# Performance work log

Measured on AMD Instinct MI355X. Metric: run time of the kernel, lower is better.

The kernel has to match this reference:

```python
import jax, jax.numpy as jnp
import numpy as np

DIM = 512
NH, NKV, HD = 8, 4, DIM // 8
KVD = NKV * HD
EPS = 1.1920928955078125e-07  # torch.finfo(float32).eps (F.rms_norm default)
ROPE_BASE = 10000.0


def _rms_norm(x):
    # F.rms_norm over last dim, no learned weight
    ms = jnp.mean(jnp.square(x), axis=-1, keepdims=True)
    return x * jax.lax.rsqrt(ms + EPS)


def _rope_tables(T, dtype):
    inv_freq = 1.0 / (ROPE_BASE ** (jnp.arange(0, HD, 2, dtype=jnp.float32) / HD))
    t = jnp.arange(T, dtype=jnp.float32)
    f = jnp.outer(t, inv_freq)  # [T, HD//2]
    return jnp.cos(f).astype(dtype)[None, None], jnp.sin(f).astype(dtype)[None, None]


def _apply_rot(x, c, s):
    h = x.shape[-1] // 2
    x1, x2 = x[..., :h], x[..., h:]
    return jnp.concatenate((x1 * c + x2 * s, -x1 * s + x2 * c), axis=-1)


def setup_inputs() -> dict:
    key = jax.random.key(0)
    ks = jax.random.split(key, 5)
    B, T = 8, 2048
    x = jax.random.normal(ks[0], (B, T, DIM), dtype=jnp.float32)
    # torch Linear weights: [out_features, in_features]
    Wq = jax.random.normal(ks[1], (DIM, DIM), dtype=jnp.float32) * (DIM ** -0.5)
    Wk = jax.random.normal(ks[2], (KVD, DIM), dtype=jnp.float32) * (DIM ** -0.5)
    Wv = jax.random.normal(ks[3], (KVD, DIM), dtype=jnp.float32) * (DIM ** -0.5)
    Wp = jax.random.normal(ks[4], (DIM, DIM), dtype=jnp.float32) * (DIM ** -0.5)
    return {"x": x, "Wq": Wq, "Wk": Wk, "Wv": Wv, "Wp": Wp}


def reference(x, Wq, Wk, Wv, Wp):
    B, T, C = x.shape
    q = (x @ Wq.T).reshape(B, T, NH, HD).transpose(0, 2, 1, 3)    # [B,NH,T,HD]
    k = (x @ Wk.T).reshape(B, T, NKV, HD).transpose(0, 2, 1, 3)   # [B,NKV,T,HD]
    v = (x @ Wv.T).reshape(B, T, NKV, HD).transpose(0, 2, 1, 3)
    q, k = _rms_norm(q), _rms_norm(k)
    c, s = _rope_tables(T, q.dtype)
    q, k = _apply_rot(q, c, s), _apply_rot(k, c, s)
    rep = NH // NKV
    k = jnp.repeat(k, rep, axis=1)  # GQA expand -> [B,NH,T,HD]
    v = jnp.repeat(v, rep, axis=1)
    scale = 1.0 / jnp.sqrt(jnp.asarray(HD, dtype=q.dtype))
    scores = jnp.einsum('bhqd,bhkd->bhqk', q, k) * scale
    causal = jnp.tril(jnp.ones((T, T), dtype=bool))
    scores = jnp.where(causal[None, None], scores, jnp.finfo(scores.dtype).min)
    attn = jax.nn.softmax(scores, axis=-1)
    y = jnp.einsum('bhqk,bhkd->bhqd', attn, v)
    y = y.transpose(0, 2, 1, 3).reshape(B, T, C)
    return y @ Wp.T
```

## Files before the change

### kernel.cpp

```cpp
#include <hip/hip_runtime.h>
#include <hip/hip_bf16.h>
#include <stdint.h>

typedef __bf16 bf16;
typedef __bf16 bf16x8 __attribute__((ext_vector_type(8)));
typedef __bf16 bf16x4 __attribute__((ext_vector_type(4)));
typedef float f32x4 __attribute__((ext_vector_type(4)));

#define T_SEQ 2048
#define DIM_ 512
#define NH_ 8
#define NKV_ 4
#define HD_ 64
#define BT_ (8 * T_SEQ)
#define NEG_INF (-1e30f)
#define EPS_ 1.1920928955078125e-07f
#define QSCALE 0.18033688011112042f
#define SMAX 12.0f

#define OFF_XB   (size_t)(0)
#define OFF_WQKV (size_t)(16777216)
#define OFF_WP   (size_t)(17825792)
#define OFF_COS  (size_t)(18350080)
#define OFF_SIN  (size_t)(18612224)
#define OFF_QT   (size_t)(18874368)
#define OFF_KT   (size_t)(35651584)
#define OFF_VT   (size_t)(44040192)
#define OFF_Y    (size_t)(52428800)
#define WS_NEEDED (size_t)(69206016)

__device__ inline void mfma16(f32x4& acc, bf16x8 a, bf16x8 b) {
    acc = __builtin_amdgcn_mfma_f32_16x16x32_bf16(a, b, acc, 0, 0, 0);
}

typedef const __attribute__((address_space(1))) uint8_t* gas_ptr;
typedef __attribute__((address_space(3))) uint8_t* las_ptr;
__device__ inline void gload16(const bf16* g, bf16* l) {
    __builtin_amdgcn_global_load_lds((gas_ptr)(const void*)g, (las_ptr)(void*)l, 16, 0, 0);
}

__global__ void prep_kernel(const float* __restrict__ x, const float* __restrict__ wq,
                            const float* __restrict__ wk, const float* __restrict__ wv,
                            const float* __restrict__ wp,
                            bf16* __restrict__ xb, bf16* __restrict__ wqkv,
                            bf16* __restrict__ wpb, float* __restrict__ cosT,
                            float* __restrict__ sinT) {
    int tid = blockIdx.x * blockDim.x + threadIdx.x;
    int stride = gridDim.x * blockDim.x;
    for (int i = tid; i < BT_ * DIM_; i += stride) xb[i] = (bf16)x[i];
    for (int i = tid; i < 1024 * 512; i += stride) {
        int j = i >> 9, k = i & 511;
        float v;
        if (j < 512) v = wq[i];
        else if (j < 768) v = wk[(j - 512) * 512 + k];
        else v = wv[(j - 768) * 512 + k];
        wqkv[i] = (bf16)v;
    }
    for (int i = tid; i < 512 * 512; i += stride) wpb[i] = (bf16)wp[i];
    for (int i = tid; i < T_SEQ * 32; i += stride) {
        int t = i >> 5, d = i & 31;
        float inv = powf(10000.0f, -(float)d * (1.0f / 32.0f));
        float f = (float)t * inv;
        cosT[i] = cosf(f);
        sinT[i] = sinf(f);
    }
}

__global__ __launch_bounds__(256) void qkv_gemm(const bf16* __restrict__ A,
                                                const bf16* __restrict__ B,
                                                bf16* __restrict__ qt,
                                                bf16* __restrict__ kt,
                                                bf16* __restrict__ vt,
                                                const float* __restrict__ cosT,
                                                const float* __restrict__ sinT) {
    __shared__ __align__(16) char smem[34816];
    bf16* As = (bf16*)smem;
    bf16* Bs = (bf16*)(smem + 16384);
    const int tid = threadIdx.x, lane = tid & 63, wid = tid >> 6;
    const int wr = wid >> 1, wc = wid & 1;
    const int lm = lane & 15, hi = lane >> 4;
    const int bid = blockIdx.x;
    const int swz = (bid & 7) * 128 + (bid >> 3);
    const int brow = (swz & 127) * 128;
    const int bcol = (swz >> 7) * 128;

    f32x4 acc[4][4] = {};
    for (int k0 = 0; k0 < 512; k0 += 64) {
        __syncthreads();
#pragma unroll
        for (int i = 0; i < 4; ++i) {
            int c = i * 256 + tid;
            int slot = c >> 6, l = c & 63;
            int row = (slot >> 1) * 16 + (l & 15);
            int kc = (slot & 1) * 32 + (l >> 4) * 8;
            gload16(A + (size_t)(brow + row) * 512 + k0 + kc, As + c * 8);
            gload16(B + (size_t)(bcol + row) * 512 + k0 + kc, Bs + c * 8);
        }
        asm volatile("s_waitcnt vmcnt(0)" ::: "memory");
        __syncthreads();
#pragma unroll
        for (int kk = 0; kk < 2; ++kk) {
            bf16x8 af[4], bfr[4];
#pragma unroll
            for (int m = 0; m < 4; ++m)
                af[m] = *(const bf16x8*)(As + (((wr * 4 + m) * 2 + kk) * 64 + lane) * 8);
#pragma unroll
            for (int n = 0; n < 4; ++n)
                bfr[n] = *(const bf16x8*)(Bs + (((wc * 4 + n) * 2 + kk) * 64 + lane) * 8);
            __builtin_amdgcn_s_setprio(1);
#pragma unroll
            for (int m = 0; m < 4; ++m)
#pragma unroll
                for (int n = 0; n < 4; ++n) mfma16(acc[m][n], af[m], bfr[n]);
            __builtin_amdgcn_s_setprio(0);
        }
    }
    __syncthreads();

    bf16* Tb = (bf16*)smem + wid * 4224;
    const int wcol = bcol + wc * 64;
    const int ctype = (wcol < 512) ? 0 : (wcol < 768 ? 1 : 2);

    if (ctype < 2) {
#pragma unroll
        for (int m = 0; m < 4; ++m)
#pragma unroll
            for (int r = 0; r < 4; ++r) {
                float v0 = acc[m][0][r], v1 = acc[m][1][r];
                float v2 = acc[m][2][r], v3 = acc[m][3][r];
                float ss = v0 * v0 + v1 * v1 + v2 * v2 + v3 * v3;
                ss += __shfl_xor(ss, 1);
                ss += __shfl_xor(ss, 2);
                ss += __shfl_xor(ss, 4);
                ss += __shfl_xor(ss, 8);
                float rinv = rsqrtf(ss * (1.0f / 64.0f) + EPS_);
                v0 *= rinv; v1 *= rinv; v2 *= rinv; v3 *= rinv;
                int rl = m * 16 + hi * 4 + r;
                int t = (brow + wr * 64 + rl) & (T_SEQ - 1);
                float c0 = cosT[t * 32 + lm], s0 = sinT[t * 32 + lm];
                float c1 = cosT[t * 32 + 16 + lm], s1 = sinT[t * 32 + 16 + lm];
                float o0 = v0 * c0 + v2 * s0;
                float o2 = v2 * c0 - v0 * s0;
                float o1 = v1 * c1 + v3 * s1;
                float o3 = v3 * c1 - v1 * s1;
                if (ctype == 0) { o0 *= QSCALE; o1 *= QSCALE; o2 *= QSCALE; o3 *= QSCALE; }
                Tb[rl * 66 + lm]      = (bf16)o0;
                Tb[rl * 66 + 16 + lm] = (bf16)o1;
                Tb[rl * 66 + 32 + lm] = (bf16)o2;
                Tb[rl * 66 + 48 + lm] = (bf16)o3;
            }
    } else {
#pragma unroll
        for (int m = 0; m < 4; ++m)
#pragma unroll
            for (int n = 0; n < 4; ++n)
#pragma unroll
                for (int r = 0; r < 4; ++r)
                    Tb[(n * 16 + lm) * 66 + m * 16 + hi * 4 + r] = (bf16)acc[m][n][r];
    }
    __syncthreads();

    const int i0 = brow + wr * 64;
    const int b = i0 >> 11, tt = i0 & (T_SEQ - 1);
#pragma unroll
    for (int p = 0; p < 8; ++p) {
        int row = p * 8 + (lane >> 3);
        int ch = lane & 7;
        bf16x8 val = *(const bf16x8*)(Tb + row * 66 + ch * 8);
        if (ctype == 0) {
            int head = wcol >> 6;
            *(bf16x8*)(qt + ((size_t)((b << 3) + head) * T_SEQ + tt + row) * 64 + ch * 8) = val;
        } else if (ctype == 1) {
            int head = (wcol - 512) >> 6;
            *(bf16x8*)(kt + ((size_t)((b << 2) + head) * T_SEQ + tt + row) * 64 + ch * 8) = val;
        } else {
            int head = (wcol - 768) >> 6;
            *(bf16x8*)(vt + ((size_t)((b << 2) + head) * 64 + row) * T_SEQ + tt + ch * 8) = val;
        }
    }
}

__global__ __launch_bounds__(256, 4) void attn_kernel(const bf16* __restrict__ qt,
                                                      const bf16* __restrict__ kt,
                                                      const bf16* __restrict__ vt,
                                                      bf16* __restrict__ y) {
    __shared__ bf16 Klds[4096];
    __shared__ bf16 Vlds[4096];
    __shared__ bf16 Plds[4][32 * 40];
    const int tid = threadIdx.x;
    const int lane = tid & 63, wid = tid >> 6;
    const int lm = lane & 15, hi = lane >> 4;
    const int bid = blockIdx.x;
    const int s4 = bid >> 8;
    const int g4 = (bid >> 6) & 3;
    const int bh = bid & 63;
    const int p = 4 * (3 - s4) + ((g4 + s4) & 3);
    const int b = bh >> 3, h = bh & 7, hv = h >> 1;
    const bf16* Q = qt + (size_t)bh * T_SEQ * HD_;
    const bf16* K = kt + (size_t)(b * NKV_ + hv) * T_SEQ * HD_;
    const bf16* V = vt + (size_t)(b * NKV_ + hv) * HD_ * T_SEQ;
    const int qB = p * 128;
    const int qw = qB + wid * 32;
    bf16* Pl = &Plds[wid][0];

    const int sl0 = tid >> 6, l0 = tid & 63;
    const int gr0 = (sl0 >> 1) * 16 + (l0 & 15);
    const int gc0 = (sl0 & 1) * 32 + (l0 >> 4) * 8;
    const int sl1 = (256 + tid) >> 6;
    const int gr1 = (sl1 >> 1) * 16 + (l0 & 15);
    const int gc1 = (sl1 & 1) * 32 + (l0 >> 4) * 8;
    const bf16* kg0 = K + (size_t)gr0 * HD_ + gc0;
    const bf16* kg1 = K + (size_t)gr1 * HD_ + gc1;
    const bf16* vg0 = V + (size_t)gr0 * T_SEQ + gc0;
    const bf16* vg1 = V + (size_t)gr1 * T_SEQ + gc1;
    bf16* kd0 = Klds + (size_t)tid * 8;
    bf16* kd1 = Klds + (size_t)(256 + tid) * 8;
    bf16* vd0 = Vlds + (size_t)tid * 8;
    bf16* vd1 = Vlds + (size_t)(256 + tid) * 8;

    bf16x8 qf[2][2];
#pragma unroll
    for (int qm = 0; qm < 2; ++qm)
#pragma unroll
        for (int kk = 0; kk < 2; ++kk)
            qf[qm][kk] = *(const bf16x8*)(Q + (size_t)(qw + 16 * qm + lm) * HD_ + 32 * kk + 8 * hi);

    f32x4 o[2][4] = {};
    float lrow[2] = {0.f, 0.f};

    const int nt = (qB >> 6) + 2;
    for (int t = 0; t < nt; ++t) {
        const int kv0 = t << 6;
        __syncthreads();
        {
            size_t ko = (size_t)kv0 * HD_, vo = (size_t)kv0;
            gload16(kg0 + ko, kd0);
            gload16(kg1 + ko, kd1);
            gload16(vg0 + vo, vd0);
            gload16(vg1 + vo, vd1);
        }
        asm volatile("s_waitcnt vmcnt(0)" ::: "memory");
        __syncthreads();

        if (kv0 <= qw + 31) {
            f32x4 s[2][4] = {};
#pragma unroll
            for (int kk = 0; kk < 2; ++kk) {
                bf16x8 kf[4];
#pragma unroll
                for (int n = 0; n < 4; ++n)
                    kf[n] = *(const bf16x8*)(Klds + ((n * 2 + kk) * 64 + lane) * 8);
#pragma unroll
                for (int qm = 0; qm < 2; ++qm)
#pragma unroll
                    for (int n = 0; n < 4; ++n) mfma16(s[qm][n], kf[n], qf[qm][kk]);
            }
            const bool partial = (kv0 + 63 > qw);
            bf16x4 pw[2][4];
#pragma unroll
            for (int qm = 0; qm < 2; ++qm) {
                const int qg = qw + 16 * qm + lm;
                float ps = 0.f;
#pragma unroll
                for (int n = 0; n < 4; ++n)
#pragma unroll
                    for (int r = 0; r < 4; ++r) {
                        float xv = s[qm][n][r];
                        if (partial)
                            xv = ((kv0 + 16 * n + 4 * hi + r) <= qg) ? xv : NEG_INF;
                        float e = __builtin_amdgcn_exp2f(xv - SMAX);
                        ps += e;
                        pw[qm][n][r] = (bf16)e;
                    }
                ps += __shfl_xor(ps, 16);
                ps += __shfl_xor(ps, 32);
                lrow[qm] += ps;
            }
#pragma unroll
            for (int kk = 0; kk < 2; ++kk) {
#pragma unroll
                for (int qm = 0; qm < 2; ++qm) {
                    *(bf16x4*)(Pl + (16 * qm + lm) * 40 + 4 * hi)      = pw[qm][2 * kk];
                    *(bf16x4*)(Pl + (16 * qm + lm) * 40 + 16 + 4 * hi) = pw[qm][2 * kk + 1];
                }
                bf16x8 vf[4], pf[2];
#pragma unroll
                for (int qm = 0; qm < 2; ++qm)
                    pf[qm] = *(const bf16x8*)(Pl + (16 * qm + lm) * 40 + 8 * hi);
#pragma unroll
                for (int nd = 0; nd < 4; ++nd)
                    vf[nd] = *(const bf16x8*)(Vlds + ((nd * 2 + kk) * 64 + lane) * 8);
#pragma unroll
                for (int qm = 0; qm < 2; ++qm)
#pragma unroll
                    for (int nd = 0; nd < 4; ++nd) mfma16(o[qm][nd], vf[nd], pf[qm]);
            }
        }
    }

#pragma unroll
    for (int qm = 0; qm < 2; ++qm) {
        float rcl = 1.0f / lrow[qm];
#pragma unroll
        for (int nd = 0; nd < 4; ++nd) {
            bf16x4 ov;
#pragma unroll
            for (int r = 0; r < 4; ++r) ov[r] = (bf16)(o[qm][nd][r] * rcl);
            *(bf16x4*)(Pl + lm * 72 + nd * 16 + 4 * hi) = ov;
        }
#pragma unroll
        for (int it = 0; it < 2; ++it) {
            int chunk = it * 64 + lane;
            int row = chunk >> 3, dc = (chunk & 7) * 8;
            bf16x8 val = *(const bf16x8*)(Pl + row * 72 + dc);
            *(bf16x8*)(y + (size_t)(b * T_SEQ + qw + 16 * qm + row) * DIM_ + h * HD_ + dc) = val;
        }
    }
}

__global__ __launch_bounds__(256) void proj_gemm(const bf16* __restrict__ A,
                                                 const bf16* __restrict__ B,
                                                 float* __restrict__ out) {
    __shared__ __align__(16) char smem[32768];
    bf16* As = (bf16*)smem;
    bf16* Bs = (bf16*)(smem + 16384);
    const int tid = threadIdx.x, lane = tid & 63, wid = tid >> 6;
    const int wr = wid >> 1, wc = wid & 1;
    const int lm = lane & 15, hi = lane >> 4;
    const int bid = blockIdx.x;
    const int swz = (bid & 7) * 64 + (bid >> 3);
    const int brow = (swz & 127) * 128;
    const int bcol = (swz >> 7) * 128;

    f32x4 acc[4][4] = {};
    for (int k0 = 0; k0 < 512; k0 += 64) {
        __syncthreads();
#pragma unroll
        for (int i = 0; i < 4; ++i) {
            int c = i * 256 + tid;
            int slot = c >> 6, l = c & 63;
            int row = (slot >> 1) * 16 + (l & 15);
            int kc = (slot & 1) * 32 + (l >> 4) * 8;
            gload16(A + (size_t)(brow + row) * 512 + k0 + kc, As + c * 8);
            gload16(B + (size_t)(bcol + row) * 512 + k0 + kc, Bs + c * 8);
        }
        asm volatile("s_waitcnt vmcnt(0)" ::: "memory");
        __syncthreads();
#pragma unroll
        for (int kk = 0; kk < 2; ++kk) {
            bf16x8 af[4], bfr[4];
#pragma unroll
            for (int m = 0; m < 4; ++m)
                af[m] = *(const bf16x8*)(As + (((wr * 4 + m) * 2 + kk) * 64 + lane) * 8);
#pragma unroll
            for (int n = 0; n < 4; ++n)
                bfr[n] = *(const bf16x8*)(Bs + (((wc * 4 + n) * 2 + kk) * 64 + lane) * 8);
            __builtin_amdgcn_s_setprio(1);
#pragma unroll
            for (int m = 0; m < 4; ++m)
#pragma unroll
                for (int n = 0; n < 4; ++n) mfma16(acc[m][n], af[m], bfr[n]);
            __builtin_amdgcn_s_setprio(0);
        }
    }
#pragma unroll
    for (int m = 0; m < 4; ++m)
#pragma unroll
        for (int n = 0; n < 4; ++n)
#pragma unroll
            for (int r = 0; r < 4; ++r) {
                int i = brow + wr * 64 + m * 16 + hi * 4 + r;
                int j = bcol + wc * 64 + n * 16 + lm;
                out[(size_t)i * DIM_ + j] = acc[m][n][r];
            }
}

extern "C" void kernel_launch(void* const* d_in, const int* in_sizes, int n_in,
                              void* d_out, int out_size, void* d_ws, size_t ws_size,
                              hipStream_t stream) {
    const float* x  = (const float*)d_in[0];
    const float* wq = (const float*)d_in[1];
    const float* wk = (const float*)d_in[2];
    const float* wv = (const float*)d_in[3];
    const float* wp = (const float*)d_in[4];
    if (ws_size < WS_NEEDED) return;

    char* ws = (char*)d_ws;
    bf16* xb    = (bf16*)(ws + OFF_XB);
    bf16* wqkv  = (bf16*)(ws + OFF_WQKV);
    bf16* wpb   = (bf16*)(ws + OFF_WP);
    float* cosT = (float*)(ws + OFF_COS);
    float* sinT = (float*)(ws + OFF_SIN);
    bf16* qt    = (bf16*)(ws + OFF_QT);
    bf16* kt    = (bf16*)(ws + OFF_KT);
    bf16* vt    = (bf16*)(ws + OFF_VT);
    bf16* y     = (bf16*)(ws + OFF_Y);

    prep_kernel<<<2048, 256, 0, stream>>>(x, wq, wk, wv, wp, xb, wqkv, wpb, cosT, sinT);

    qkv_gemm<<<1024, 256, 0, stream>>>(xb, wqkv, qt, kt, vt, cosT, sinT);

    attn_kernel<<<dim3(16 * 64), 256, 0, stream>>>(qt, kt, vt, y);

    proj_gemm<<<512, 256, 0, stream>>>(y, wpb, (float*)d_out);
}
```

Measured before the change: 152.4 us.

## Halve attention query tile to 64 rows and compute row sums via MFMA

The attention kernel now processes 64 query rows per block (16 per wave) instead of 128, doubling the grid to 2048 blocks, with a remapped tile ordering that still schedules heavy causal tiles first. The softmax row sum is now accumulated by an extra MFMA against a vector of ones instead of scalar adds and cross-lane shuffles. The aim is better load balance and occupancy on the causal workload and fewer VALU and shuffle instructions. In exchange, K/V tiles are loaded into LDS twice as often per query row, and the row sum is taken from bf16-rounded probabilities.

```diff
diff --git a/kernel.cpp b/kernel.cpp
--- a/kernel.cpp
+++ b/kernel.cpp
@@ -186,21 +186,21 @@
                                                       bf16* __restrict__ y) {
     __shared__ bf16 Klds[4096];
     __shared__ bf16 Vlds[4096];
-    __shared__ bf16 Plds[4][32 * 40];
+    __shared__ bf16 Plds[4][1152];
     const int tid = threadIdx.x;
     const int lane = tid & 63, wid = tid >> 6;
     const int lm = lane & 15, hi = lane >> 4;
     const int bid = blockIdx.x;
-    const int s4 = bid >> 8;
+    const int s8 = bid >> 8;
     const int g4 = (bid >> 6) & 3;
     const int bh = bid & 63;
-    const int p = 4 * (3 - s4) + ((g4 + s4) & 3);
+    const int p = 4 * (7 - s8) + ((g4 + s8) & 3);
     const int b = bh >> 3, h = bh & 7, hv = h >> 1;
     const bf16* Q = qt + (size_t)bh * T_SEQ * HD_;
     const bf16* K = kt + (size_t)(b * NKV_ + hv) * T_SEQ * HD_;
     const bf16* V = vt + (size_t)(b * NKV_ + hv) * HD_ * T_SEQ;
-    const int qB = p * 128;
-    const int qw = qB + wid * 32;
+    const int qB = p * 64;
+    const int qw = qB + wid * 16;
     bf16* Pl = &Plds[wid][0];
 
     const int sl0 = tid >> 6, l0 = tid & 63;
@@ -218,17 +218,19 @@
     bf16* vd0 = Vlds + (size_t)tid * 8;
     bf16* vd1 = Vlds + (size_t)(256 + tid) * 8;
 
-    bf16x8 qf[2][2];
-#pragma unroll
-    for (int qm = 0; qm < 2; ++qm)
-#pragma unroll
-        for (int kk = 0; kk < 2; ++kk)
-            qf[qm][kk] = *(const bf16x8*)(Q + (size_t)(qw + 16 * qm + lm) * HD_ + 32 * kk + 8 * hi);
-
-    f32x4 o[2][4] = {};
-    float lrow[2] = {0.f, 0.f};
-
-    const int nt = (qB >> 6) + 2;
+    bf16x8 qf[2];
+#pragma unroll
+    for (int kk = 0; kk < 2; ++kk)
+        qf[kk] = *(const bf16x8*)(Q + (size_t)(qw + lm) * HD_ + 32 * kk + 8 * hi);
+
+    bf16x8 vones;
+#pragma unroll
+    for (int j = 0; j < 8; ++j) vones[j] = (bf16)1.0f;
+
+    f32x4 o[4] = {};
+    f32x4 lacc = {};
+
+    const int nt = p + 1;
     for (int t = 0; t < nt; ++t) {
         const int kv0 = t << 6;
         __syncthreads();
@@ -242,8 +244,8 @@
         asm volatile("s_waitcnt vmcnt(0)" ::: "memory");
         __syncthreads();
 
-        if (kv0 <= qw + 31) {
-            f32x4 s[2][4] = {};
+        if (kv0 <= qw + 15) {
+            f32x4 s[4] = {};
 #pragma unroll
             for (int kk = 0; kk < 2; ++kk) {
                 bf16x8 kf[4];
@@ -251,70 +253,50 @@
                 for (int n = 0; n < 4; ++n)
                     kf[n] = *(const bf16x8*)(Klds + ((n * 2 + kk) * 64 + lane) * 8);
 #pragma unroll
-                for (int qm = 0; qm < 2; ++qm)
-#pragma unroll
-                    for (int n = 0; n < 4; ++n) mfma16(s[qm][n], kf[n], qf[qm][kk]);
+                for (int n = 0; n < 4; ++n) mfma16(s[n], kf[n], qf[kk]);
             }
             const bool partial = (kv0 + 63 > qw);
-            bf16x4 pw[2][4];
-#pragma unroll
-            for (int qm = 0; qm < 2; ++qm) {
-                const int qg = qw + 16 * qm + lm;
-                float ps = 0.f;
-#pragma unroll
-                for (int n = 0; n < 4; ++n)
-#pragma unroll
-                    for (int r = 0; r < 4; ++r) {
-                        float xv = s[qm][n][r];
-                        if (partial)
-                            xv = ((kv0 + 16 * n + 4 * hi + r) <= qg) ? xv : NEG_INF;
-                        float e = __builtin_amdgcn_exp2f(xv - SMAX);
-                        ps += e;
-                        pw[qm][n][r] = (bf16)e;
-                    }
-                ps += __shfl_xor(ps, 16);
-                ps += __shfl_xor(ps, 32);
-                lrow[qm] += ps;
-            }
+            const int qg = qw + lm;
+            bf16x4 pw[4];
+#pragma unroll
+            for (int n = 0; n < 4; ++n)
+#pragma unroll
+                for (int r = 0; r < 4; ++r) {
+                    float xv = s[n][r];
+                    if (partial)
+                        xv = ((kv0 + 16 * n + 4 * hi + r) <= qg) ? xv : NEG_INF;
+                    pw[n][r] = (bf16)__builtin_amdgcn_exp2f(xv - SMAX);
+                }
 #pragma unroll
             for (int kk = 0; kk < 2; ++kk) {
-#pragma unroll
-                for (int qm = 0; qm < 2; ++qm) {
-                    *(bf16x4*)(Pl + (16 * qm + lm) * 40 + 4 * hi)      = pw[qm][2 * kk];
-                    *(bf16x4*)(Pl + (16 * qm + lm) * 40 + 16 + 4 * hi) = pw[qm][2 * kk + 1];
-                }
-                bf16x8 vf[4], pf[2];
-#pragma unroll
-                for (int qm = 0; qm < 2; ++qm)
-                    pf[qm] = *(const bf16x8*)(Pl + (16 * qm + lm) * 40 + 8 * hi);
+                *(bf16x4*)(Pl + lm * 40 + 4 * hi)      = pw[2 * kk];
+                *(bf16x4*)(Pl + lm * 40 + 16 + 4 * hi) = pw[2 * kk + 1];
+                bf16x8 vf[4], pf;
+                pf = *(const bf16x8*)(Pl + lm * 40 + 8 * hi);
 #pragma unroll
                 for (int nd = 0; nd < 4; ++nd)
                     vf[nd] = *(const bf16x8*)(Vlds + ((nd * 2 + kk) * 64 + lane) * 8);
 #pragma unroll
-                for (int qm = 0; qm < 2; ++qm)
-#pragma unroll
-                    for (int nd = 0; nd < 4; ++nd) mfma16(o[qm][nd], vf[nd], pf[qm]);
+                for (int nd = 0; nd < 4; ++nd) mfma16(o[nd], vf[nd], pf);
+                mfma16(lacc, vones, pf);
             }
         }
     }
 
-#pragma unroll
-    for (int qm = 0; qm < 2; ++qm) {
-        float rcl = 1.0f / lrow[qm];
-#pragma unroll
-        for (int nd = 0; nd < 4; ++nd) {
-            bf16x4 ov;
-#pragma unroll
-            for (int r = 0; r < 4; ++r) ov[r] = (bf16)(o[qm][nd][r] * rcl);
-            *(bf16x4*)(Pl + lm * 72 + nd * 16 + 4 * hi) = ov;
-        }
-#pragma unroll
-        for (int it = 0; it < 2; ++it) {
-            int chunk = it * 64 + lane;
-            int row = chunk >> 3, dc = (chunk & 7) * 8;
-            bf16x8 val = *(const bf16x8*)(Pl + row * 72 + dc);
-            *(bf16x8*)(y + (size_t)(b * T_SEQ + qw + 16 * qm + row) * DIM_ + h * HD_ + dc) = val;
-        }
+    float rcl = 1.0f / lacc[0];
+#pragma unroll
+    for (int nd = 0; nd < 4; ++nd) {
+        bf16x4 ov;
+#pragma unroll
+        for (int r = 0; r < 4; ++r) ov[r] = (bf16)(o[nd][r] * rcl);
+        *(bf16x4*)(Pl + lm * 72 + nd * 16 + 4 * hi) = ov;
+    }
+#pragma unroll
+    for (int it = 0; it < 2; ++it) {
+        int chunk = it * 64 + lane;
+        int row = chunk >> 3, dc = (chunk & 7) * 8;
+        bf16x8 val = *(const bf16x8*)(Pl + row * 72 + dc);
+        *(bf16x8*)(y + (size_t)(b * T_SEQ + qw + row) * DIM_ + h * HD_ + dc) = val;
     }
 }
 
@@ -400,7 +382,7 @@
 
     qkv_gemm<<<1024, 256, 0, stream>>>(xb, wqkv, qt, kt, vt, cosT, sinT);
 
-    attn_kernel<<<dim3(16 * 64), 256, 0, stream>>>(qt, kt, vt, y);
+    attn_kernel<<<2048, 256, 0, stream>>>(qt, kt, vt, y);
 
     proj_gemm<<<512, 256, 0, stream>>>(y, wpb, (float*)d_out);
 }
```

Measured after the change: 147.7 us. 3.1% less time.
